# Optimization experiments

Measured on AMD Instinct MI355X. Metric: run time of the kernel, lower is better.

## Reference

```python
import jax, jax.numpy as jnp
import numpy as np

DIM = 2048
N_HEADS = 16
N_KV_HEADS = 4
ROPE_BASE = 10000.0
QK_GAIN_INIT = 1.0
B, T = 4, 2048


def setup_inputs() -> dict:
    key = jax.random.key(0)
    ks = jax.random.split(key, 5)
    head_dim = DIM // N_HEADS
    kv_dim = N_KV_HEADS * head_dim
    x = jax.random.normal(ks[0], (B, T, DIM), dtype=jnp.float32)
    wq = jax.random.normal(ks[1], (DIM, DIM), dtype=jnp.float32) * 0.02
    wk = jax.random.normal(ks[2], (kv_dim, DIM), dtype=jnp.float32) * 0.02
    wv = jax.random.normal(ks[3], (kv_dim, DIM), dtype=jnp.float32) * 0.02
    wo = jax.random.normal(ks[4], (DIM, DIM), dtype=jnp.float32) * 0.02
    q_gain = jnp.full((N_HEADS,), QK_GAIN_INIT, dtype=jnp.float32)
    k_gain = jnp.full((N_KV_HEADS,), QK_GAIN_INIT, dtype=jnp.float32)
    return {"x": x, "wq": wq, "wk": wk, "wv": wv, "wo": wo,
            "q_gain": q_gain, "k_gain": k_gain}


def _rope_tables(T, head_dim, dtype):
    # inv_freq over even indices, freqs = outer(t, inv_freq) -> [T, head_dim//2]
    inv_freq = ROPE_BASE ** (-jnp.arange(0, head_dim, 2, dtype=jnp.float32) / head_dim)
    freqs = jnp.arange(T, dtype=jnp.float32)[:, None] * inv_freq[None, :]
    return jnp.cos(freqs).astype(dtype), jnp.sin(freqs).astype(dtype)


def _apply_rotary(x, cos, sin):
    # x: [..., T, head_dim]; cos/sin: [T, head_dim//2] broadcast over leading dims
    half = x.shape[-1] // 2
    x1, x2 = x[..., :half], x[..., half:]
    return jnp.concatenate((x1 * cos + x2 * sin, -x1 * sin + x2 * cos), axis=-1)


def reference(x, wq, wk, wv, wo, q_gain, k_gain):
    Bx, Tx, C = x.shape
    H, KV = N_HEADS, N_KV_HEADS
    D = C // H
    G = H // KV  # query groups per kv head

    q = (x @ wq.T).reshape(Bx, Tx, H, D)    # [B,T,H,D]
    k = (x @ wk.T).reshape(Bx, Tx, KV, D)   # [B,T,KV,D]
    v = (x @ wv.T).reshape(Bx, Tx, KV, D)

    q = q * q_gain[None, None, :, None]
    k = k * k_gain[None, None, :, None]

    cos, sin = _rope_tables(Tx, D, x.dtype)
    q = _apply_rotary(q.transpose(0, 2, 1, 3), cos, sin)  # [B,H,T,D]
    k = _apply_rotary(k.transpose(0, 2, 1, 3), cos, sin)  # [B,KV,T,D]
    v = v.transpose(0, 2, 1, 3)                            # [B,KV,T,D]

    # GQA without materializing repeated k/v: group query heads per kv head
    q = q.reshape(Bx, KV, G, Tx, D)
    scale = 1.0 / jnp.sqrt(jnp.array(D, dtype=x.dtype))
    scores = jnp.einsum('bkgtd,bksd->bkgts', q, k) * scale  # [B,KV,G,T,T]
    causal = jnp.tril(jnp.ones((Tx, Tx), dtype=bool))
    scores = jnp.where(causal, scores, jnp.finfo(scores.dtype).min)
    attn = jax.nn.softmax(scores, axis=-1)
    y = jnp.einsum('bkgts,bksd->bkgtd', attn, v)            # [B,KV,G,T,D]
    y = y.reshape(Bx, H, Tx, D).transpose(0, 2, 1, 3).reshape(Bx, Tx, C)
    return y @ wo.T
```

## Files before the change

### kernel.cpp

```cpp
#include <hip/hip_runtime.h>
#include <hip/hip_bf16.h>

typedef __bf16 bf16x8 __attribute__((ext_vector_type(8)));
typedef float f32x4 __attribute__((ext_vector_type(4)));

#define DIMC 2048
#define HD   128
#define NH   16
#define NKV  4
#define BSZ  4
#define TSZ  2048
#define MROWS (BSZ * TSZ)
#define NQKV  (DIMC + 2 * NKV * HD)


__device__ __forceinline__ void async_copy16(const void* g, void* l) {
  __builtin_amdgcn_global_load_lds(
      (const __attribute__((address_space(1))) void*)g,
      (__attribute__((address_space(3))) void*)l, 16, 0, 0);
}


__global__ void cvt_all(const float* __restrict__ x, const float* __restrict__ wq,
                        const float* __restrict__ wk, const float* __restrict__ wv,
                        const float* __restrict__ wo, __hip_bfloat16* __restrict__ dst) {
  const long n0 = (long)MROWS * DIMC;
  const long n1 = n0 + (long)DIMC * DIMC;
  const long n2 = n1 + (long)NKV * HD * DIMC;
  const long n3 = n2 + (long)NKV * HD * DIMC;
  long i = ((long)blockIdx.x * blockDim.x + threadIdx.x) * 4;
  const float* src; long off;
  if (i < n0)      { src = x;  off = i; }
  else if (i < n1) { src = wq; off = i - n0; }
  else if (i < n2) { src = wk; off = i - n1; }
  else if (i < n3) { src = wv; off = i - n2; }
  else             { src = wo; off = i - n3; }
  float4 v = *(const float4*)(src + off);
  union { __hip_bfloat16 b[4]; short4 s; } u;
  u.b[0] = __float2bfloat16(v.x);
  u.b[1] = __float2bfloat16(v.y);
  u.b[2] = __float2bfloat16(v.z);
  u.b[3] = __float2bfloat16(v.w);
  *(short4*)(dst + i) = u.s;
}


__global__ void rope_tab(float* __restrict__ ct, float* __restrict__ st) {
  int idx = blockIdx.x * blockDim.x + threadIdx.x;
  int d = idx & 63, t = idx >> 6;
  float inv = powf(10000.0f, -(float)d * (1.0f / 64.0f));
  float f = (float)t * inv;
  ct[idx] = cosf(f);
  st[idx] = sinf(f);
}


__device__ __forceinline__ void load_frags4(const __hip_bfloat16* p, int rbase,
                                            int quad, int l7, int l15,
                                            bf16x8 fr[4][2]) {
#pragma unroll
  for (int i = 0; i < 4; i++) {
    const int r = rbase + i * 16 + l15;
#pragma unroll
    for (int kk = 0; kk < 2; kk++)
      fr[i][kk] = *(const bf16x8*)&p[r * 64 + (((kk << 2) + quad) ^ l7) * 8];
  }
}

__device__ __forceinline__ void mfma_quad(f32x4 acc[8][4], const bf16x8 a[4][2],
                                          const bf16x8 b[4][2], int mb, int nb) {
#pragma unroll
  for (int kk = 0; kk < 2; kk++)
#pragma unroll
    for (int mi = 0; mi < 4; mi++)
#pragma unroll
      for (int ni = 0; ni < 2; ni++)
        acc[mb + mi][nb + ni] = __builtin_amdgcn_mfma_f32_16x16x32_bf16(
            a[mi][kk], b[nb + ni][kk], acc[mb + mi][nb + ni], 0, 0, 0);
}

template <int OUT_BF16>
__global__ __launch_bounds__(512, 2) void gemm256_bt(
    const __hip_bfloat16* __restrict__ A, const __hip_bfloat16* __restrict__ Bw,
    void* __restrict__ Cv, int M, int N, int K) {
  __shared__ __align__(16) __hip_bfloat16 lsA[2][16384];
  __shared__ __align__(16) __hip_bfloat16 lsB[2][16384];
  const int tid = threadIdx.x;
  const int w = tid >> 6, lane = tid & 63;
  const int quad = lane >> 4, l15 = lane & 15, l7 = lane & 7;
  const int wr = w >> 2, wc = w & 3;
  const int wrow = wr * 128, wcol = wc * 64;
  const int wbase = w * 512;

  const int nwg = gridDim.x * gridDim.y;
  const int bid = blockIdx.y * gridDim.x + blockIdx.x;
  const int sw = (bid & 7) * (nwg >> 3) + (bid >> 3);
  const int m0 = (sw / gridDim.x) * 256, n0 = (sw % gridDim.x) * 256;

  const int NTt = K >> 6;

  const __hip_bfloat16 *gA0, *gA1, *gB0, *gB1;
  {
    const int p0 = tid, p1 = 512 + tid;
    const int r0 = p0 >> 3, c0 = ((p0 & 7) ^ (r0 & 7)) * 8;
    const int r1 = p1 >> 3, c1 = ((p1 & 7) ^ (r1 & 7)) * 8;
    gA0 = A + (long)(m0 + r0) * K + c0;
    gA1 = A + (long)(m0 + r1) * K + c1;
    gB0 = Bw + (long)(n0 + r0) * K + c0;
    gB1 = Bw + (long)(n0 + r1) * K + c1;
  }
  const long hstep = (long)128 * K;

  auto stage_half = [&](int st) {
    if (st >= 4 * NTt) return;
    const int t2 = st >> 2, hf = st & 3;
    const long koff = (long)(t2 << 6);
    if (hf < 2) {
      __hip_bfloat16* L = &lsB[t2 & 1][hf * 8192 + wbase];
      const long o = (long)hf * hstep + koff;
      async_copy16(gB0 + o, L);
      async_copy16(gB1 + o, L + 4096);
    } else {
      __hip_bfloat16* L = &lsA[t2 & 1][(hf - 2) * 8192 + wbase];
      const long o = (long)(hf - 2) * hstep + koff;
      async_copy16(gA0 + o, L);
      async_copy16(gA1 + o, L + 4096);
    }
  };

  f32x4 acc[8][4] = {};
  bf16x8 a[4][2], b[4][2];

#pragma unroll
  for (int st = 0; st < 7; st++) stage_half(st);
  asm volatile("s_waitcnt vmcnt(6)" ::: "memory");
  __builtin_amdgcn_s_barrier();

  for (int t = 0; t < NTt; t++) {
    const __hip_bfloat16* pA = lsA[t & 1];
    const __hip_bfloat16* pB = lsB[t & 1];

    load_frags4(pA, wrow, quad, l7, l15, a);
    load_frags4(pB, wcol, quad, l7, l15, b);
    stage_half(4 * t + 7);
    asm volatile("s_waitcnt lgkmcnt(8)" ::: "memory");
    __builtin_amdgcn_s_barrier();
    asm volatile("s_waitcnt lgkmcnt(0)" ::: "memory");
    __builtin_amdgcn_s_setprio(1);
    mfma_quad(acc, a, b, 0, 0);
    __builtin_amdgcn_s_setprio(0);
    __builtin_amdgcn_s_barrier();

    stage_half(4 * t + 8);
    __builtin_amdgcn_s_barrier();
    __builtin_amdgcn_s_setprio(1);
    mfma_quad(acc, a, b, 0, 2);
    __builtin_amdgcn_s_setprio(0);
    __builtin_amdgcn_s_barrier();

    load_frags4(pA, wrow + 64, quad, l7, l15, a);
    stage_half(4 * t + 9);
    __builtin_amdgcn_s_barrier();
    asm volatile("s_waitcnt lgkmcnt(0)" ::: "memory");
    __builtin_amdgcn_s_setprio(1);
    mfma_quad(acc, a, b, 4, 0);
    __builtin_amdgcn_s_setprio(0);
    __builtin_amdgcn_s_barrier();

    stage_half(4 * t + 10);
    __builtin_amdgcn_s_barrier();
    __builtin_amdgcn_s_setprio(1);
    mfma_quad(acc, a, b, 4, 2);
    __builtin_amdgcn_s_setprio(0);
    if (t < NTt - 3) asm volatile("s_waitcnt vmcnt(6)" ::: "memory");
    else             asm volatile("s_waitcnt vmcnt(0)" ::: "memory");
    __builtin_amdgcn_s_barrier();
  }

#pragma unroll
  for (int mi = 0; mi < 8; mi++) {
#pragma unroll
    for (int r = 0; r < 4; r++) {
      const long row = m0 + wrow + mi * 16 + quad * 4 + r;
      if (OUT_BF16) {
        __hip_bfloat16* Cb = (__hip_bfloat16*)Cv;
#pragma unroll
        for (int ni = 0; ni < 4; ni++)
          Cb[row * N + n0 + wcol + ni * 16 + l15] = __float2bfloat16(acc[mi][ni][r]);
      } else {
        float* Cf = (float*)Cv;
#pragma unroll
        for (int ni = 0; ni < 4; ni++)
          Cf[row * N + n0 + wcol + ni * 16 + l15] = acc[mi][ni][r];
      }
    }
  }
}


__global__ void rope_apply(const __hip_bfloat16* __restrict__ qkv,
                           const float* __restrict__ ct, const float* __restrict__ st,
                           const float* __restrict__ qg, const float* __restrict__ kg,
                           __hip_bfloat16* __restrict__ qr, __hip_bfloat16* __restrict__ kr) {
  const long QN = (long)BSZ * TSZ * NH * 64;
  long idx = (long)blockIdx.x * blockDim.x + threadIdx.x;
  if (idx < QN) {
    int d = idx & 63;
    int h = (int)((idx >> 6) & 15);
    long bt = idx >> 10;
    int t = (int)(bt & (TSZ - 1));
    long base = bt * NQKV + h * HD + d;
    float x1 = __bfloat162float(qkv[base]);
    float x2 = __bfloat162float(qkv[base + 64]);
    float c = ct[t * 64 + d], s = st[t * 64 + d];
    float g = qg[h] * 0.08838834764831845f * 1.4426950408889634f;
    long ob = ((bt >> 11) * NH + h) * ((long)TSZ * HD) + (long)t * HD + d;
    qr[ob]      = __float2bfloat16((x1 * c + x2 * s) * g);
    qr[ob + 64] = __float2bfloat16((-x1 * s + x2 * c) * g);
  } else {
    long j = idx - QN;
    int d = (int)(j & 63);
    int kv = (int)((j >> 6) & 3);
    long bt = j >> 8;
    int t = (int)(bt & (TSZ - 1));
    long base = bt * NQKV + DIMC + kv * HD + d;
    float x1 = __bfloat162float(qkv[base]);
    float x2 = __bfloat162float(qkv[base + 64]);
    float c = ct[t * 64 + d], s = st[t * 64 + d];
    float g = kg[kv];
    long ob = ((bt >> 11) * NKV + kv) * ((long)TSZ * HD) + (long)t * HD + d;
    kr[ob]      = __float2bfloat16((x1 * c + x2 * s) * g);
    kr[ob + 64] = __float2bfloat16((-x1 * s + x2 * c) * g);
  }
}


__global__ void vtrans(const __hip_bfloat16* __restrict__ qkv, __hip_bfloat16* __restrict__ vt) {
  __shared__ __hip_bfloat16 tile[64][65];
  const int bkv = blockIdx.z;
  const int b = bkv >> 2, kv = bkv & 3;
  const int t0 = blockIdx.y * 64, d0 = blockIdx.x * 64;
  const int tx = threadIdx.x, ty = threadIdx.y;
#pragma unroll
  for (int i = 0; i < 8; i++) {
    int t = ty + i * 8;
    tile[t][tx] = qkv[(long)(b * TSZ + t0 + t) * NQKV + DIMC + NKV * HD + kv * HD + d0 + tx];
  }
  __syncthreads();
#pragma unroll
  for (int i = 0; i < 8; i++) {
    int d = ty + i * 8;
    vt[((long)((b * NKV + kv) * HD + d0 + d)) * TSZ + t0 + tx] = tile[tx][d];
  }
}


__global__ __launch_bounds__(256, 2) void attn(
    const __hip_bfloat16* __restrict__ Q, const __hip_bfloat16* __restrict__ Kr,
    const __hip_bfloat16* __restrict__ Vt, __hip_bfloat16* __restrict__ Y) {
  __shared__ __align__(16) __hip_bfloat16 lds_v[2][64 * 128];
  __shared__ __align__(16) __hip_bfloat16 lds_k[64 * 128];
  __shared__ __align__(16) __hip_bfloat16 lds_p[4][32 * 64];
  const int qpair = blockIdx.x, bh = blockIdx.y;
  const int b = bh >> 4, h = bh & 15, kv = h >> 2;
  const int tid = threadIdx.x, wave = tid >> 6, lane = tid & 63;
  const int quad = lane >> 4, l15 = lane & 15, l7 = lane & 7;
  const __hip_bfloat16* Kp = Kr + (long)(b * NKV + kv) * TSZ * HD;
  const __hip_bfloat16* Vp = Vt + (long)(b * NKV + kv) * HD * TSZ;

  union { short u[8]; bf16x8 v; } ones;
#pragma unroll
  for (int i = 0; i < 8; i++) ones.u[i] = 0x3F80;

  auto stageK = [&](int j) {
#pragma unroll
    for (int i = 0; i < 4; i++) {
      int p = (i * 4 + wave) * 64 + lane;
      int row = p >> 4;
      int gc = (p & 15) ^ (row & 7);
      async_copy16(Kp + (long)j * 8192 + row * 128 + gc * 8, &lds_k[(i * 4 + wave) * 512]);
    }
  };
  auto stageV = [&](int j, int buf) {
#pragma unroll
    for (int i = 0; i < 4; i++) {
      int p = (i * 4 + wave) * 64 + lane;
      int d = p >> 3;
      int gc = (p & 7) ^ (d & 7);
      async_copy16(Vp + (long)d * TSZ + j * 64 + gc * 8, &lds_v[buf][(i * 4 + wave) * 512]);
    }
  };

  for (int half = 0; half < 2; half++) {
    const int qi = half ? (15 - qpair) : qpair;
    const __hip_bfloat16* Qp = Q + ((long)(b * NH + h) * TSZ + qi * 128 + wave * 32) * HD;
    bf16x8 aq[2][4];
#pragma unroll
    for (int ni = 0; ni < 2; ni++)
#pragma unroll
      for (int kk = 0; kk < 4; kk++)
        aq[ni][kk] = *(const bf16x8*)&Qp[(ni * 16 + l15) * HD + kk * 32 + quad * 8];

    f32x4 o[2][8] = {};
    f32x4 osum[2] = {};
    const int njt = 2 * qi + 2;

    stageV(0, 0);
    stageK(0);
    for (int j = 0; j < njt; j++) {
      __syncthreads();
      if (j + 1 < njt) stageV(j + 1, (j + 1) & 1);

      f32x4 s[4][2] = {};
#pragma unroll
      for (int kk = 0; kk < 4; kk++) {
        bf16x8 bk[4];
#pragma unroll
        for (int mi = 0; mi < 4; mi++)
          bk[mi] = *(const bf16x8*)&lds_k[(mi * 16 + l15) * 128 + ((kk * 4 + quad) ^ l7) * 8];
#pragma unroll
        for (int mi = 0; mi < 4; mi++)
#pragma unroll
          for (int ni = 0; ni < 2; ni++)
            s[mi][ni] = __builtin_amdgcn_mfma_f32_16x16x32_bf16(bk[mi], aq[ni][kk], s[mi][ni], 0, 0, 0);
      }

      const bool diag = (j >= 2 * qi);
#pragma unroll
      for (int mi = 0; mi < 4; mi++) {
#pragma unroll
        for (int ni = 0; ni < 2; ni++) {
          f32x4 p4;
          if (diag) {
            int qrow = qi * 128 + wave * 32 + ni * 16 + l15;
            int kbase = j * 64 + mi * 16 + quad * 4;
#pragma unroll
            for (int r = 0; r < 4; r++)
              p4[r] = (kbase + r <= qrow) ? exp2f(s[mi][ni][r]) : 0.f;
          } else {
#pragma unroll
            for (int r = 0; r < 4; r++) p4[r] = exp2f(s[mi][ni][r]);
          }
          const int c = mi * 4 + quad;
          const int addr = (ni * 16 + l15) * 64 + (((c >> 1) ^ l7) * 2 + (c & 1)) * 4;
          union { __hip_bfloat162 h2[2]; uint2 u; } pk;
          pk.h2[0] = __float22bfloat162_rn(float2{p4[0], p4[1]});
          pk.h2[1] = __float22bfloat162_rn(float2{p4[2], p4[3]});
          *(uint2*)&lds_p[wave][addr] = pk.u;
        }
      }

      asm volatile("s_barrier" ::: "memory");
      if (j + 1 < njt) stageK(j + 1);
      asm volatile("s_waitcnt lgkmcnt(0)" ::: "memory");

      const __hip_bfloat16* lv = lds_v[j & 1];
#pragma unroll
      for (int kk = 0; kk < 2; kk++) {
        bf16x8 ap[2];
#pragma unroll
        for (int mi = 0; mi < 2; mi++)
          ap[mi] = *(const bf16x8*)&lds_p[wave][(mi * 16 + l15) * 64 + ((kk * 4 + quad) ^ l7) * 8];
#pragma unroll
        for (int mi = 0; mi < 2; mi++)
          osum[mi] = __builtin_amdgcn_mfma_f32_16x16x32_bf16(ap[mi], ones.v, osum[mi], 0, 0, 0);
#pragma unroll
        for (int nd = 0; nd < 8; nd++) {
          bf16x8 bv = *(const bf16x8*)&lv[(nd * 16 + l15) * 64 + ((kk * 4 + quad) ^ l7) * 8];
#pragma unroll
          for (int mi = 0; mi < 2; mi++)
            o[mi][nd] = __builtin_amdgcn_mfma_f32_16x16x32_bf16(ap[mi], bv, o[mi][nd], 0, 0, 0);
        }
      }
    }

    const long yb0 = (long)b * TSZ + qi * 128 + wave * 32;
#pragma unroll
    for (int mi = 0; mi < 2; mi++) {
#pragma unroll
      for (int r = 0; r < 4; r++) {
        float inv = 1.0f / osum[mi][r];
        long row = yb0 + mi * 16 + quad * 4 + r;
#pragma unroll
        for (int nd = 0; nd < 8; nd++)
          Y[row * DIMC + h * HD + nd * 16 + l15] = __float2bfloat16(o[mi][nd][r] * inv);
      }
    }
    __syncthreads();
  }
}


extern "C" void kernel_launch(void* const* d_in, const int* in_sizes, int n_in,
                              void* d_out, int out_size, void* d_ws, size_t ws_size,
                              hipStream_t stream) {
  const float* x  = (const float*)d_in[0];
  const float* wq = (const float*)d_in[1];
  const float* wk = (const float*)d_in[2];
  const float* wv = (const float*)d_in[3];
  const float* wo = (const float*)d_in[4];
  const float* qg = (const float*)d_in[5];
  const float* kg = (const float*)d_in[6];

  char* ws = (char*)d_ws;
  size_t off = 0;
  auto alloc = [&](size_t bytes) {
    char* p = ws + off;
    off += (bytes + 255) & ~(size_t)255;
    return p;
  };
  __hip_bfloat16* xb    = (__hip_bfloat16*)alloc((size_t)MROWS * DIMC * 2);
  __hip_bfloat16* wqkvb = (__hip_bfloat16*)alloc((size_t)NQKV * DIMC * 2);
  __hip_bfloat16* wob   = (__hip_bfloat16*)alloc((size_t)DIMC * DIMC * 2);
  __hip_bfloat16* qkv   = (__hip_bfloat16*)alloc((size_t)MROWS * NQKV * 2);
  __hip_bfloat16* qr    = (__hip_bfloat16*)alloc((size_t)MROWS * DIMC * 2);
  __hip_bfloat16* kr    = (__hip_bfloat16*)alloc((size_t)BSZ * NKV * TSZ * HD * 2);
  __hip_bfloat16* vt    = (__hip_bfloat16*)alloc((size_t)BSZ * NKV * TSZ * HD * 2);
  float* ct = (float*)alloc((size_t)TSZ * 64 * 4);
  float* st = (float*)alloc((size_t)TSZ * 64 * 4);
  __hip_bfloat16* yb = xb;

  const long NCVT = (long)MROWS * DIMC + (long)DIMC * DIMC * 2 + (long)NKV * HD * DIMC * 2;
  cvt_all<<<NCVT / 1024, 256, 0, stream>>>(x, wq, wk, wv, wo, xb);
  rope_tab<<<TSZ * 64 / 256, 256, 0, stream>>>(ct, st);

  gemm256_bt<1><<<dim3(NQKV / 256, MROWS / 256), 512, 0, stream>>>(xb, wqkvb, qkv, MROWS, NQKV, DIMC);

  const long QN = (long)BSZ * TSZ * NH * 64;
  const long KN = (long)BSZ * TSZ * NKV * 64;
  rope_apply<<<(QN + KN) / 256, 256, 0, stream>>>(qkv, ct, st, qg, kg, qr, kr);
  vtrans<<<dim3(HD / 64, TSZ / 64, BSZ * NKV), dim3(64, 8), 0, stream>>>(qkv, vt);

  attn<<<dim3(8, BSZ * NH), 256, 0, stream>>>(qr, kr, vt, yb);

  gemm256_bt<0><<<dim3(DIMC / 256, MROWS / 256), 512, 0, stream>>>(yb, wob, d_out, MROWS, DIMC, DIMC);
}
```

Baseline: 456.8 us.

## Restructure GEMM main loop with register double-buffered fragments and cross-tile prefetch

The 256x256 bf16 GEMM main loop is rescheduled. Each wave now holds two A-fragment sets and two half-width B-fragment sets, so the next tile's first fragments load from LDS while the current tile's last MFMA quadrant runs. Global-to-LDS staging changes from quarter-tile granularity to whole A and B tiles, issued at different points in the loop. There are fewer barriers per iteration, and the lgkmcnt waits are replaced by vmcnt waits. This aims to hide LDS latency and barrier stalls. It costs more registers and relies on subtle correctness of the vmcnt counts and LDS buffer reuse.

```diff
diff --git a/kernel.cpp b/kernel.cpp
--- a/kernel.cpp
+++ b/kernel.cpp
@@ -55,9 +55,8 @@
 }
 
 
-__device__ __forceinline__ void load_frags4(const __hip_bfloat16* p, int rbase,
-                                            int quad, int l7, int l15,
-                                            bf16x8 fr[4][2]) {
+__device__ __forceinline__ void loadA4(const __hip_bfloat16* p, int rbase,
+                                       int quad, int l7, int l15, bf16x8 fr[4][2]) {
 #pragma unroll
   for (int i = 0; i < 4; i++) {
     const int r = rbase + i * 16 + l15;
@@ -67,8 +66,19 @@
   }
 }
 
-__device__ __forceinline__ void mfma_quad(f32x4 acc[8][4], const bf16x8 a[4][2],
-                                          const bf16x8 b[4][2], int mb, int nb) {
+__device__ __forceinline__ void loadB2(const __hip_bfloat16* p, int rbase,
+                                       int quad, int l7, int l15, bf16x8 fr[2][2]) {
+#pragma unroll
+  for (int i = 0; i < 2; i++) {
+    const int r = rbase + i * 16 + l15;
+#pragma unroll
+    for (int kk = 0; kk < 2; kk++)
+      fr[i][kk] = *(const bf16x8*)&p[r * 64 + (((kk << 2) + quad) ^ l7) * 8];
+  }
+}
+
+__device__ __forceinline__ void mq(f32x4 acc[8][4], const bf16x8 a[4][2],
+                                   const bf16x8 b[2][2], int mb, int nb) {
 #pragma unroll
   for (int kk = 0; kk < 2; kk++)
 #pragma unroll
@@ -76,7 +86,7 @@
 #pragma unroll
       for (int ni = 0; ni < 2; ni++)
         acc[mb + mi][nb + ni] = __builtin_amdgcn_mfma_f32_16x16x32_bf16(
-            a[mi][kk], b[nb + ni][kk], acc[mb + mi][nb + ni], 0, 0, 0);
+            a[mi][kk], b[ni][kk], acc[mb + mi][nb + ni], 0, 0, 0);
 }
 
 template <int OUT_BF16>
@@ -111,68 +121,69 @@
   }
   const long hstep = (long)128 * K;
 
-  auto stage_half = [&](int st) {
-    if (st >= 4 * NTt) return;
-    const int t2 = st >> 2, hf = st & 3;
+  auto stageA2 = [&](int t2) {
+    if (t2 >= NTt) return;
+    __hip_bfloat16* L = &lsA[t2 & 1][wbase];
     const long koff = (long)(t2 << 6);
-    if (hf < 2) {
-      __hip_bfloat16* L = &lsB[t2 & 1][hf * 8192 + wbase];
-      const long o = (long)hf * hstep + koff;
-      async_copy16(gB0 + o, L);
-      async_copy16(gB1 + o, L + 4096);
-    } else {
-      __hip_bfloat16* L = &lsA[t2 & 1][(hf - 2) * 8192 + wbase];
-      const long o = (long)(hf - 2) * hstep + koff;
-      async_copy16(gA0 + o, L);
-      async_copy16(gA1 + o, L + 4096);
-    }
+    async_copy16(gA0 + koff, L);
+    async_copy16(gA1 + koff, L + 4096);
+    async_copy16(gA0 + hstep + koff, L + 8192);
+    async_copy16(gA1 + hstep + koff, L + 8192 + 4096);
   };
+  auto stageB2 = [&](int t2) {
+    if (t2 >= NTt) return;
+    __hip_bfloat16* L = &lsB[t2 & 1][wbase];
+    const long koff = (long)(t2 << 6);
+    async_copy16(gB0 + koff, L);
+    async_copy16(gB1 + koff, L + 4096);
+    async_copy16(gB0 + hstep + koff, L + 8192);
+    async_copy16(gB1 + hstep + koff, L + 8192 + 4096);
+  };
 
   f32x4 acc[8][4] = {};
-  bf16x8 a[4][2], b[4][2];
-
-#pragma unroll
-  for (int st = 0; st < 7; st++) stage_half(st);
-  asm volatile("s_waitcnt vmcnt(6)" ::: "memory");
+  bf16x8 a0[4][2], a1[4][2], b0[2][2], b1[2][2];
+
+  stageA2(0); stageB2(0); stageA2(1); stageB2(1);
+  asm volatile("s_waitcnt vmcnt(8)" ::: "memory");
   __builtin_amdgcn_s_barrier();
+  loadA4(lsA[0], wrow, quad, l7, l15, a0);
+  loadB2(lsB[0], wcol, quad, l7, l15, b0);
 
   for (int t = 0; t < NTt; t++) {
     const __hip_bfloat16* pA = lsA[t & 1];
     const __hip_bfloat16* pB = lsB[t & 1];
 
-    load_frags4(pA, wrow, quad, l7, l15, a);
-    load_frags4(pB, wcol, quad, l7, l15, b);
-    stage_half(4 * t + 7);
-    asm volatile("s_waitcnt lgkmcnt(8)" ::: "memory");
-    __builtin_amdgcn_s_barrier();
-    asm volatile("s_waitcnt lgkmcnt(0)" ::: "memory");
+    loadA4(pA, wrow + 64, quad, l7, l15, a1);
+    loadB2(pB, wcol + 32, quad, l7, l15, b1);
     __builtin_amdgcn_s_setprio(1);
-    mfma_quad(acc, a, b, 0, 0);
+    mq(acc, a0, b0, 0, 0);
     __builtin_amdgcn_s_setprio(0);
     __builtin_amdgcn_s_barrier();
 
-    stage_half(4 * t + 8);
-    __builtin_amdgcn_s_barrier();
     __builtin_amdgcn_s_setprio(1);
-    mfma_quad(acc, a, b, 0, 2);
+    mq(acc, a1, b0, 4, 0);
     __builtin_amdgcn_s_setprio(0);
     __builtin_amdgcn_s_barrier();
 
-    load_frags4(pA, wrow + 64, quad, l7, l15, a);
-    stage_half(4 * t + 9);
+    stageA2(t + 2);
+    __builtin_amdgcn_s_setprio(1);
+    mq(acc, a0, b1, 0, 2);
+    __builtin_amdgcn_s_setprio(0);
+    if (t < NTt - 2) asm volatile("s_waitcnt vmcnt(6)" ::: "memory");
+    else             asm volatile("s_waitcnt vmcnt(0)" ::: "memory");
     __builtin_amdgcn_s_barrier();
-    asm volatile("s_waitcnt lgkmcnt(0)" ::: "memory");
+
+    stageB2(t + 2);
+    if (t + 1 < NTt) {
+      const __hip_bfloat16* qA = lsA[(t + 1) & 1];
+      const __hip_bfloat16* qB = lsB[(t + 1) & 1];
+      loadA4(qA, wrow, quad, l7, l15, a0);
+      loadB2(qB, wcol, quad, l7, l15, b0);
+    }
     __builtin_amdgcn_s_setprio(1);
-    mfma_quad(acc, a, b, 4, 0);
+    mq(acc, a1, b1, 4, 2);
     __builtin_amdgcn_s_setprio(0);
-    __builtin_amdgcn_s_barrier();
-
-    stage_half(4 * t + 10);
-    __builtin_amdgcn_s_barrier();
-    __builtin_amdgcn_s_setprio(1);
-    mfma_quad(acc, a, b, 4, 2);
-    __builtin_amdgcn_s_setprio(0);
-    if (t < NTt - 3) asm volatile("s_waitcnt vmcnt(6)" ::: "memory");
+    if (t < NTt - 2) asm volatile("s_waitcnt vmcnt(8)" ::: "memory");
     else             asm volatile("s_waitcnt vmcnt(0)" ::: "memory");
     __builtin_amdgcn_s_barrier();
   }
```

Result: slower. 477.3 us (+4.5%).
